# Optimization experiments

Measured on AMD Instinct MI355X. Metric: run time of the kernel, lower is better.

Reference implementation:

```python
import jax, jax.numpy as jnp
import numpy as np

NH, WS, SS = 8, 7, 3  # num_heads, window_size, shift_size
EPS = 1e-5


def _rel_pos_index(ws):
    coords = np.stack(np.meshgrid(np.arange(ws), np.arange(ws), indexing='ij'))
    coords = coords.reshape(2, -1)                      # [2, L]
    rel = coords[:, :, None] - coords[:, None, :]       # [2, L, L]
    rel = rel.transpose(1, 2, 0) + (ws - 1)
    return rel[..., 0] * (2 * ws - 1) + rel[..., 1]     # [L, L] int


def _attn_mask(H, W, ws, ss):
    # region labels for shifted-window masking (torchvision semantics)
    img = np.zeros((H, W))
    slices = (slice(0, -ws), slice(-ws, -ss), slice(-ss, None))
    cnt = 0
    for hs in slices:
        for wsl in slices:
            img[hs, wsl] = cnt
            cnt += 1
    win = img.reshape(H // ws, ws, W // ws, ws).transpose(0, 2, 1, 3).reshape(-1, ws * ws)
    mask = (win[:, None, :] != win[:, :, None]).astype(np.float32) * (-100.0)
    return mask  # [nWin, L, L]


def _layernorm(x, gamma, beta):
    mu = jnp.mean(x, axis=-1, keepdims=True)
    var = jnp.mean(jnp.square(x - mu), axis=-1, keepdims=True)
    return (x - mu) * jax.lax.rsqrt(var + EPS) * gamma + beta


def _swin_attention(x, qkv_w, qkv_b, proj_w, proj_b, rpb_table):
    B, H, W, C = x.shape
    HD = C // NH
    L = WS * WS
    nH, nW = H // WS, W // WS
    # cyclic shift
    xs = jnp.roll(x, shift=(-SS, -SS), axis=(1, 2))
    # window partition -> [B*nWin, L, C]
    xw = xs.reshape(B, nH, WS, nW, WS, C).transpose(0, 1, 3, 2, 4, 5).reshape(B * nH * nW, L, C)
    qkv = jnp.einsum('nlc,dc->nld', xw, qkv_w) + qkv_b
    qkv = qkv.reshape(-1, L, 3, NH, HD).transpose(2, 0, 3, 1, 4)  # [3, N, h, L, d]
    q, k, v = qkv[0] * (HD ** -0.5), qkv[1], qkv[2]
    attn = jnp.einsum('nhid,nhjd->nhij', q, k)  # [N, h, L, L]
    bias = rpb_table[jnp.asarray(_rel_pos_index(WS))]  # [L, L, h]
    attn = attn + bias.transpose(2, 0, 1)[None]
    mask = jnp.asarray(_attn_mask(H, W, WS, SS))  # [nWin, L, L]
    nwin = nH * nW
    attn = attn.reshape(B, nwin, NH, L, L) + mask[None, :, None]
    attn = jax.nn.softmax(attn.reshape(-1, NH, L, L), axis=-1)
    out = jnp.einsum('nhij,nhjd->nhid', attn, v).transpose(0, 2, 1, 3).reshape(-1, L, C)
    out = jnp.einsum('nlc,dc->nld', out, proj_w) + proj_b
    # reverse windows and shift
    out = out.reshape(B, nH, nW, WS, WS, C).transpose(0, 1, 3, 2, 4, 5).reshape(B, H, W, C)
    return jnp.roll(out, shift=(SS, SS), axis=(1, 2))


def setup_inputs() -> dict:
    key = jax.random.key(0)
    ks = jax.random.split(key, 8)
    B, H, W, C = 32, 56, 56, 256
    F = 4 * C
    s = 0.02
    return {
        'x': jax.random.normal(ks[0], (B, H, W, C), jnp.float32),
        'qkv_w': jax.random.normal(ks[1], (3 * C, C), jnp.float32) * s,
        'qkv_b': jnp.zeros((3 * C,), jnp.float32),
        'proj_w': jax.random.normal(ks[2], (C, C), jnp.float32) * s,
        'proj_b': jnp.zeros((C,), jnp.float32),
        'rpb_table': jax.random.normal(ks[3], ((2 * WS - 1) ** 2, NH), jnp.float32) * s,
        'gamma1': jnp.ones((C,), jnp.float32),
        'beta1': jnp.zeros((C,), jnp.float32),
        'w1': jax.random.normal(ks[4], (C, F), jnp.float32) * s,
        'b1': jax.random.normal(ks[5], (F,), jnp.float32) * 1e-6,
        'w2': jax.random.normal(ks[6], (F, C), jnp.float32) * s,
        'b2': jax.random.normal(ks[7], (C,), jnp.float32) * 1e-6,
        'gamma2': jnp.ones((C,), jnp.float32),
        'beta2': jnp.zeros((C,), jnp.float32),
    }


def reference(x, qkv_w, qkv_b, proj_w, proj_b, rpb_table, gamma1, beta1, w1, b1, w2, b2, gamma2, beta2):
    # post-norm residual block: x + norm1(attn(x)); x + norm2(mlp(x))
    a = _swin_attention(x, qkv_w, qkv_b, proj_w, proj_b, rpb_table)
    x = x + _layernorm(a, gamma1, beta1)
    h = jax.nn.gelu(jnp.einsum('bhwc,cf->bhwf', x, w1) + b1, approximate=False)
    m = jnp.einsum('bhwf,fc->bhwc', h, w2) + b2
    x = x + _layernorm(m, gamma2, beta2)
    return x
```

## Files before the change

### kernel.cpp

```cpp
#include <hip/hip_runtime.h>
#include <hip/hip_bf16.h>


typedef unsigned short ushort_t;
typedef short bf16x8 __attribute__((ext_vector_type(8)));
typedef float f32x4 __attribute__((ext_vector_type(4)));

#define WAITV0 asm volatile("s_waitcnt vmcnt(0)" ::: "memory")
#define WAITV3 asm volatile("s_waitcnt vmcnt(3)" ::: "memory")
#define WAITV4 asm volatile("s_waitcnt vmcnt(4)" ::: "memory")
#define WAITV5 asm volatile("s_waitcnt vmcnt(5)" ::: "memory")
#define WAITL0 asm volatile("s_waitcnt lgkmcnt(0)" ::: "memory")
#define BAR    __builtin_amdgcn_s_barrier()

__device__ __forceinline__ float bf2f(unsigned short u) {
    union { unsigned int i; float f; } x; x.i = ((unsigned int)u) << 16; return x.f;
}
__device__ __forceinline__ unsigned short f2bf(float f) {
    union { float f; unsigned int i; } x; x.f = f;
    unsigned int r = x.i + 0x7fffu + ((x.i >> 16) & 1u);
    return (unsigned short)(r >> 16);
}
__device__ __forceinline__ bf16x8 pack8(float4 a, float4 b) {
    bf16x8 r;
    r[0] = (short)f2bf(a.x); r[1] = (short)f2bf(a.y);
    r[2] = (short)f2bf(a.z); r[3] = (short)f2bf(a.w);
    r[4] = (short)f2bf(b.x); r[5] = (short)f2bf(b.y);
    r[6] = (short)f2bf(b.z); r[7] = (short)f2bf(b.w);
    return r;
}
__device__ __forceinline__ void gl_lds16(const ushort_t* g, ushort_t* l) {
    __builtin_amdgcn_global_load_lds((const __attribute__((address_space(1))) void*)g,
                                     (__attribute__((address_space(3))) void*)l, 16, 0, 0);
}
__device__ __forceinline__ float gelu_f(float v) {
    float s = v * 0.70710678118654752f;
    float ax = fabsf(s);
    float t = __builtin_amdgcn_rcpf(1.0f + 0.3275911f * ax);
    float poly = ((((1.061405429f * t - 1.453152027f) * t + 1.421413741f) * t
                   - 0.284496736f) * t + 0.254829592f) * t;
    float y = 1.0f - poly * __expf(-ax * ax);
    float e = (s < 0.f) ? -y : y;
    return 0.5f * v * (1.0f + e);
}

__device__ __forceinline__ long swin_src_off(int m) {
    int n = m / 49, l = m - n * 49;
    int b = n >> 6, win = n & 63;
    int wh = win >> 3, ww = win & 7;
    int i = l / 7, j = l - i * 7;
    int hs = wh * 7 + i + 3; if (hs >= 56) hs -= 56;
    int ws = ww * 7 + j + 3; if (ws >= 56) ws -= 56;
    return ((long)(b * 56 + hs) * 56 + ws) * 256;
}

template<int SRCT>
__global__ __launch_bounds__(256)
void convW(const float* __restrict__ src, ushort_t* __restrict__ dst, int N, int kshift)
{
    int idx = blockIdx.x * 256 + threadIdx.x;
    int kk = idx & ((1 << kshift) - 1), nn = idx >> kshift;
    float v = SRCT ? src[(long)kk * N + nn] : src[idx];
    dst[idx] = f2bf(v);
}

template<int ACT, int AMODE, int NCOLS>
__global__ __launch_bounds__(512)
void gemmW(const void* __restrict__ Av, const ushort_t* __restrict__ W,
           const float* __restrict__ bias, ushort_t* __restrict__ C,
           int M, int N, int K)
{
    constexpr int NA = (AMODE == 1) ? 2 : 3;
    __shared__ ushort_t As[NA * 4096];
    __shared__ ushort_t Bs[3 * 8192];
    const int t = threadIdx.x, lane = t & 63, w = t >> 6;
    const int cpx = gridDim.x >> 3;
    const int wg = (blockIdx.x & 7) * cpx + (blockIdx.x >> 3);
    const int row0 = (wg / NCOLS) * 128, col0 = (wg % NCOLS) * 256;
    const int wm = (w >> 2) * 64, wn = (w & 3) * 64;

    const int ra = t >> 2, sa = ((t & 3) ^ ((ra >> 1) & 3)) * 8;
    const ushort_t* ag = nullptr;
    const float* axr = nullptr;
    if (AMODE == 0) ag = (const ushort_t*)Av + (long)(row0 + ra) * K + sa;
    else            axr = (const float*)Av + swin_src_off(row0 + ra) + sa;

    const int ub0 = t, ub1 = t + 512;
    const int rb0 = ub0 >> 2, sb0 = ((ub0 & 3) ^ ((rb0 >> 1) & 3)) * 8;
    const int rb1 = ub1 >> 2, sb1 = ((ub1 & 3) ^ ((rb1 >> 1) & 3)) * 8;
    const ushort_t* bg0 = W + (long)(col0 + rb0) * K + sb0;
    const ushort_t* bg1 = W + (long)(col0 + rb1) * K + sb1;

    int offA[4], offB[4];
    #pragma unroll
    for (int i = 0; i < 4; i++) {
        int r2 = wm + i * 16 + (lane & 15);
        offA[i] = r2 * 32 + (((lane >> 4) ^ ((r2 >> 1) & 3)) * 8);
        int r3 = wn + i * 16 + (lane & 15);
        offB[i] = r3 * 32 + (((lane >> 4) ^ ((r3 >> 1) & 3)) * 8);
    }

    f32x4 acc[4][4] = {};
    float4 va0, vb0, va1, vb1;

    if (AMODE == 0) {
        gl_lds16(ag,      &As[t * 8]);
        gl_lds16(bg0,      &Bs[ub0 * 8]);
        gl_lds16(bg1,      &Bs[ub1 * 8]);
        gl_lds16(ag + 32, &As[4096 + t * 8]);
        gl_lds16(bg0 + 32, &Bs[8192 + ub0 * 8]);
        gl_lds16(bg1 + 32, &Bs[8192 + ub1 * 8]);
        WAITV3; BAR;
    } else {
        va0 = *(const float4*)axr;        vb0 = *(const float4*)(axr + 4);
        gl_lds16(bg0,      &Bs[ub0 * 8]);
        gl_lds16(bg1,      &Bs[ub1 * 8]);
        va1 = *(const float4*)(axr + 32); vb1 = *(const float4*)(axr + 36);
        gl_lds16(bg0 + 32, &Bs[8192 + ub0 * 8]);
        gl_lds16(bg1 + 32, &Bs[8192 + ub1 * 8]);
        WAITV4;
        *(bf16x8*)&As[t * 8] = pack8(va0, vb0);
        WAITL0; BAR;
    }

    const int nk = K >> 5;
    int i0 = 0, i1 = 1, i2 = 2;
    for (int kt = 0; kt < nk; kt++) {
        const bool more = (kt + 2 < nk);
        if (more) {
            const int k2 = (kt + 2) * 32;
            if (AMODE == 0) {
                gl_lds16(ag + k2, &As[i2 * 4096 + t * 8]);
            } else {
                if (kt & 1) { va1 = *(const float4*)(axr + k2); vb1 = *(const float4*)(axr + k2 + 4); }
                else        { va0 = *(const float4*)(axr + k2); vb0 = *(const float4*)(axr + k2 + 4); }
            }
            gl_lds16(bg0 + k2, &Bs[i2 * 8192 + ub0 * 8]);
            gl_lds16(bg1 + k2, &Bs[i2 * 8192 + ub1 * 8]);
        }
        {
            const int abase = (AMODE == 1 ? (kt & 1) : i0) * 4096;
            const int bbase = i0 * 8192;
            bf16x8 af[4], bw[4];
            #pragma unroll
            for (int i = 0; i < 4; i++) {
                af[i] = *(const bf16x8*)&As[abase + offA[i]];
                bw[i] = *(const bf16x8*)&Bs[bbase + offB[i]];
            }
            #pragma unroll
            for (int mi = 0; mi < 4; mi++)
                #pragma unroll
                for (int ni = 0; ni < 4; ni++)
                    acc[mi][ni] = __builtin_amdgcn_mfma_f32_16x16x32_bf16(af[mi], bw[ni], acc[mi][ni], 0, 0, 0);
        }
        if (kt < nk - 1) {
            if (AMODE == 0) {
                if (more) { WAITV3; } else { WAITV0; }
            } else {
                if (more) { WAITV4; } else { WAITV0; }
                if (kt & 1) *(bf16x8*)&As[t * 8]        = pack8(va0, vb0);
                else        *(bf16x8*)&As[4096 + t * 8] = pack8(va1, vb1);
                WAITL0;
            }
            BAR;
        }
        int tmp = i0; i0 = i1; i1 = i2; i2 = tmp;
    }

    #pragma unroll
    for (int mi = 0; mi < 4; mi++)
        #pragma unroll
        for (int ni = 0; ni < 4; ni++) {
            const int c = col0 + wn + ni * 16 + (lane & 15);
            const float bv = bias[c];
            #pragma unroll
            for (int r = 0; r < 4; r++) {
                const int rr = row0 + wm + mi * 16 + (lane >> 4) * 4 + r;
                float v = acc[mi][ni][r] + bv;
                if (ACT) v = gelu_f(v);
                C[(long)rr * N + c] = f2bf(v);
            }
        }
}

__global__ __launch_bounds__(64)
void attn_mfma(const ushort_t* __restrict__ qkv, const float* __restrict__ rpb,
               ushort_t* __restrict__ out)
{
    __shared__ ushort_t v_t[32 * 72];
    __shared__ ushort_t p_lds[64 * 72];
    __shared__ float bias_s[169];

    const int blk = blockIdx.x;
    const int n = blk >> 3, h = blk & 7;
    const int l = threadIdx.x;
    const long wbase = (long)n * 49 * 768 + h * 32;
    const float scale = 0.17677669529663687f;

    {
        int j = min(l, 48);
        const ushort_t* vr = qkv + wbase + (long)j * 768 + 512;
        #pragma unroll
        for (int c = 0; c < 4; c++) {
            bf16x8 vv = *(const bf16x8*)(vr + c * 8);
            #pragma unroll
            for (int e = 0; e < 8; e++) v_t[(c * 8 + e) * 72 + l] = (ushort_t)vv[e];
        }
    }
    for (int idx = l; idx < 169; idx += 64) bias_s[idx] = rpb[idx * 8 + h];
    __syncthreads();

    f32x4 s[4][4] = {};
    {
        bf16x8 aq[4], bk[4];
        #pragma unroll
        for (int mt = 0; mt < 4; mt++) {
            int i = min(mt * 16 + (l & 15), 48);
            aq[mt] = *(const bf16x8*)(qkv + wbase + (long)i * 768 + (l >> 4) * 8);
        }
        #pragma unroll
        for (int nt = 0; nt < 4; nt++) {
            int j = min(nt * 16 + (l & 15), 48);
            bk[nt] = *(const bf16x8*)(qkv + wbase + (long)j * 768 + 256 + (l >> 4) * 8);
        }
        #pragma unroll
        for (int mt = 0; mt < 4; mt++)
            #pragma unroll
            for (int nt = 0; nt < 4; nt++)
                s[mt][nt] = __builtin_amdgcn_mfma_f32_16x16x32_bf16(aq[mt], bk[nt], s[mt][nt], 0, 0, 0);
    }

    const int win = n & 63, wh = win >> 3, ww = win & 7;
    int yj[4], xj[4], regj[4]; bool jv[4];
    #pragma unroll
    for (int nt = 0; nt < 4; nt++) {
        int j = nt * 16 + (l & 15);
        jv[nt] = (j <= 48);
        int jc = min(j, 48);
        yj[nt] = jc / 7; xj[nt] = jc - yj[nt] * 7;
        int hs = wh * 7 + yj[nt], wsx = ww * 7 + xj[nt];
        regj[nt] = (hs < 49 ? 0 : (hs < 53 ? 1 : 2)) * 3 + (wsx < 49 ? 0 : (wsx < 53 ? 1 : 2));
    }
    float rinv[4][4];
    #pragma unroll
    for (int mt = 0; mt < 4; mt++) {
        #pragma unroll
        for (int r = 0; r < 4; r++) {
            int i = mt * 16 + (l >> 4) * 4 + r;
            int ic = min(i, 48);
            int yi = ic / 7, xi = ic - yi * 7;
            int hs = wh * 7 + yi, wsx = ww * 7 + xi;
            int regi = (hs < 49 ? 0 : (hs < 53 ? 1 : 2)) * 3 + (wsx < 49 ? 0 : (wsx < 53 ? 1 : 2));
            float val[4];
            #pragma unroll
            for (int nt = 0; nt < 4; nt++) {
                float v = s[mt][nt][r] * scale + bias_s[(yi - yj[nt] + 6) * 13 + (xi - xj[nt] + 6)];
                if (regi != regj[nt]) v -= 100.f;
                val[nt] = jv[nt] ? v : -1e30f;
            }
            float mx = fmaxf(fmaxf(val[0], val[1]), fmaxf(val[2], val[3]));
            #pragma unroll
            for (int off = 1; off <= 8; off <<= 1) mx = fmaxf(mx, __shfl_xor(mx, off));
            float sum = 0.f;
            #pragma unroll
            for (int nt = 0; nt < 4; nt++) { val[nt] = __expf(val[nt] - mx); sum += val[nt]; }
            #pragma unroll
            for (int off = 1; off <= 8; off <<= 1) sum += __shfl_xor(sum, off);
            rinv[mt][r] = 1.0f / sum;
            #pragma unroll
            for (int nt = 0; nt < 4; nt++)
                p_lds[i * 72 + nt * 16 + (l & 15)] = f2bf(val[nt]);
        }
    }
    __syncthreads();

    f32x4 o[4][2] = {};
    #pragma unroll
    for (int ks = 0; ks < 2; ks++) {
        bf16x8 pa[4], vb[2];
        #pragma unroll
        for (int mt = 0; mt < 4; mt++)
            pa[mt] = *(const bf16x8*)&p_lds[(mt * 16 + (l & 15)) * 72 + ks * 32 + (l >> 4) * 8];
        #pragma unroll
        for (int nt = 0; nt < 2; nt++)
            vb[nt] = *(const bf16x8*)&v_t[(nt * 16 + (l & 15)) * 72 + ks * 32 + (l >> 4) * 8];
        #pragma unroll
        for (int mt = 0; mt < 4; mt++)
            #pragma unroll
            for (int nt = 0; nt < 2; nt++)
                o[mt][nt] = __builtin_amdgcn_mfma_f32_16x16x32_bf16(pa[mt], vb[nt], o[mt][nt], 0, 0, 0);
    }
    #pragma unroll
    for (int mt = 0; mt < 4; mt++)
        #pragma unroll
        for (int r = 0; r < 4; r++) {
            int i = mt * 16 + (l >> 4) * 4 + r;
            if (i < 49) {
                float rs = rinv[mt][r];
                #pragma unroll
                for (int nt = 0; nt < 2; nt++) {
                    int d = nt * 16 + (l & 15);
                    out[((long)n * 49 + i) * 256 + h * 32 + d] = f2bf(o[mt][nt][r] * rs);
                }
            }
        }
}

__global__ __launch_bounds__(512)
void projln1(const ushort_t* __restrict__ A, const ushort_t* __restrict__ W,
             const float* __restrict__ pb, const float* __restrict__ x,
             const float* __restrict__ gamma, const float* __restrict__ beta,
             ushort_t* __restrict__ x1b)
{
    __shared__ ushort_t As[3 * 4096];
    __shared__ ushort_t Bs[3 * 8192];
    __shared__ float red_s[128][4];
    __shared__ float red_ss[128][4];
    __shared__ int srow_s[128];
    const int t = threadIdx.x, lane = t & 63, w = t >> 6;
    const int row0 = blockIdx.x * 128;
    const int wm = (w >> 2) * 64, wn = (w & 3) * 64;

    if (t < 128) srow_s[t] = (int)(swin_src_off(row0 + t) >> 8);

    const int ra0 = t >> 2, sa0 = ((t & 3) ^ ((ra0 >> 1) & 3)) * 8;
    const ushort_t* ag = A + (long)(row0 + ra0) * 256 + sa0;
    const int ub0 = t, ub1 = t + 512;
    const int rb0 = ub0 >> 2, sb0 = ((ub0 & 3) ^ ((rb0 >> 1) & 3)) * 8;
    const int rb1 = ub1 >> 2, sb1 = ((ub1 & 3) ^ ((rb1 >> 1) & 3)) * 8;
    const ushort_t* bg0 = W + (long)rb0 * 256 + sb0;
    const ushort_t* bg1 = W + (long)rb1 * 256 + sb1;

    int offA[4], offB[4];
    #pragma unroll
    for (int i = 0; i < 4; i++) {
        int ra = wm + i * 16 + (lane & 15);
        offA[i] = ra * 32 + (((lane >> 4) ^ ((ra >> 1) & 3)) * 8);
        int rb = wn + i * 16 + (lane & 15);
        offB[i] = rb * 32 + (((lane >> 4) ^ ((rb >> 1) & 3)) * 8);
    }

    f32x4 acc[4][4] = {};
    gl_lds16(ag,       &As[t * 8]);
    gl_lds16(bg0,       &Bs[ub0 * 8]);
    gl_lds16(bg1,       &Bs[ub1 * 8]);
    gl_lds16(ag + 32,  &As[4096 + t * 8]);
    gl_lds16(bg0 + 32,  &Bs[8192 + ub0 * 8]);
    gl_lds16(bg1 + 32,  &Bs[8192 + ub1 * 8]);
    WAITV3; BAR;

    int i0 = 0, i1 = 1, i2 = 2;
    for (int kt = 0; kt < 8; kt++) {
        const bool more = (kt + 2 < 8);
        if (more) {
            const int k2 = (kt + 2) * 32;
            gl_lds16(ag + k2, &As[i2 * 4096 + t * 8]);
            gl_lds16(bg0 + k2, &Bs[i2 * 8192 + ub0 * 8]);
            gl_lds16(bg1 + k2, &Bs[i2 * 8192 + ub1 * 8]);
        }
        bf16x8 af[4], bw[4];
        #pragma unroll
        for (int i = 0; i < 4; i++) {
            af[i] = *(const bf16x8*)&As[i0 * 4096 + offA[i]];
            bw[i] = *(const bf16x8*)&Bs[i0 * 8192 + offB[i]];
        }
        #pragma unroll
        for (int mi = 0; mi < 4; mi++)
            #pragma unroll
            for (int ni = 0; ni < 4; ni++)
                acc[mi][ni] = __builtin_amdgcn_mfma_f32_16x16x32_bf16(af[mi], bw[ni], acc[mi][ni], 0, 0, 0);
        if (kt < 7) {
            if (more) { WAITV3; } else { WAITV0; }
            BAR;
        }
        int tmp = i0; i0 = i1; i1 = i2; i2 = tmp;
    }

    float pbv[4], g1v[4], be1v[4];
    #pragma unroll
    for (int ni = 0; ni < 4; ni++) {
        int col = wn + ni * 16 + (lane & 15);
        pbv[ni] = pb[col]; g1v[ni] = gamma[col]; be1v[ni] = beta[col];
    }
    #pragma unroll
    for (int mi = 0; mi < 4; mi++)
        #pragma unroll
        for (int rr = 0; rr < 4; rr++) {
            float s = 0.f, ss = 0.f;
            #pragma unroll
            for (int ni = 0; ni < 4; ni++) {
                float v = acc[mi][ni][rr] + pbv[ni];
                acc[mi][ni][rr] = v; s += v; ss += v * v;
            }
            #pragma unroll
            for (int off = 1; off <= 8; off <<= 1) { s += __shfl_xor(s, off); ss += __shfl_xor(ss, off); }
            if ((lane & 15) == 0) {
                int r = wm + mi * 16 + (lane >> 4) * 4 + rr;
                red_s[r][w & 3] = s; red_ss[r][w & 3] = ss;
            }
        }
    __syncthreads();
    #pragma unroll
    for (int mi = 0; mi < 4; mi++)
        #pragma unroll
        for (int rr = 0; rr < 4; rr++) {
            const int r = wm + mi * 16 + (lane >> 4) * 4 + rr;
            const float s = red_s[r][0] + red_s[r][1] + red_s[r][2] + red_s[r][3];
            const float ss = red_ss[r][0] + red_ss[r][1] + red_ss[r][2] + red_ss[r][3];
            const float mu = s * (1.0f / 256.0f);
            const float rstd = rsqrtf(ss * (1.0f / 256.0f) - mu * mu + 1e-5f);
            const long sp = srow_s[r];
            #pragma unroll
            for (int ni = 0; ni < 4; ni++) {
                int col = wn + ni * 16 + (lane & 15);
                float o = x[sp * 256 + col] + (acc[mi][ni][rr] - mu) * rstd * g1v[ni] + be1v[ni];
                x1b[sp * 256 + col] = f2bf(o);
            }
        }
}

__global__ __launch_bounds__(256)
void mlp2ln2(const ushort_t* __restrict__ A, const ushort_t* __restrict__ W,
             const float* __restrict__ pb, const ushort_t* __restrict__ x1res,
             const float* __restrict__ gamma, const float* __restrict__ beta,
             float* __restrict__ out)
{
    __shared__ ushort_t As[3 * 2048];
    __shared__ ushort_t Bs[3 * 8192];
    __shared__ float red_s[64][4];
    __shared__ float red_ss[64][4];
    const int t = threadIdx.x, lane = t & 63, w = t >> 6;
    const int row0 = blockIdx.x * 64;
    const int wn = w * 64;

    const int ra0 = t >> 2, sa0 = ((t & 3) ^ ((ra0 >> 1) & 3)) * 8;
    const ushort_t* ag = A + (long)(row0 + ra0) * 1024 + sa0;
    const ushort_t* bg[4];
    int ub[4];
    #pragma unroll
    for (int i = 0; i < 4; i++) {
        ub[i] = t + i * 256;
        int rb = ub[i] >> 2, sb = ((ub[i] & 3) ^ ((rb >> 1) & 3)) * 8;
        bg[i] = W + (long)rb * 1024 + sb;
    }

    int offA[4], offB[4];
    #pragma unroll
    for (int i = 0; i < 4; i++) {
        int ra = i * 16 + (lane & 15);
        offA[i] = ra * 32 + (((lane >> 4) ^ ((ra >> 1) & 3)) * 8);
        int rb = wn + i * 16 + (lane & 15);
        offB[i] = rb * 32 + (((lane >> 4) ^ ((rb >> 1) & 3)) * 8);
    }

    f32x4 acc[4][4] = {};
    gl_lds16(ag,      &As[t * 8]);
    #pragma unroll
    for (int i = 0; i < 4; i++) gl_lds16(bg[i],      &Bs[ub[i] * 8]);
    gl_lds16(ag + 32, &As[2048 + t * 8]);
    #pragma unroll
    for (int i = 0; i < 4; i++) gl_lds16(bg[i] + 32, &Bs[8192 + ub[i] * 8]);
    WAITV5; BAR;

    int i0 = 0, i1 = 1, i2 = 2;
    for (int kt = 0; kt < 32; kt++) {
        const bool more = (kt + 2 < 32);
        if (more) {
            const int k2 = (kt + 2) * 32;
            gl_lds16(ag + k2, &As[i2 * 2048 + t * 8]);
            #pragma unroll
            for (int i = 0; i < 4; i++) gl_lds16(bg[i] + k2, &Bs[i2 * 8192 + ub[i] * 8]);
        }
        bf16x8 af[4], bw[4];
        #pragma unroll
        for (int i2x = 0; i2x < 4; i2x++) {
            af[i2x] = *(const bf16x8*)&As[i0 * 2048 + offA[i2x]];
            bw[i2x] = *(const bf16x8*)&Bs[i0 * 8192 + offB[i2x]];
        }
        #pragma unroll
        for (int mi = 0; mi < 4; mi++)
            #pragma unroll
            for (int ni = 0; ni < 4; ni++)
                acc[mi][ni] = __builtin_amdgcn_mfma_f32_16x16x32_bf16(af[mi], bw[ni], acc[mi][ni], 0, 0, 0);
        if (kt < 31) {
            if (more) { WAITV5; } else { WAITV0; }
            BAR;
        }
        int tmp = i0; i0 = i1; i1 = i2; i2 = tmp;
    }

    float pbv[4], g2v[4], be2v[4];
    #pragma unroll
    for (int ni = 0; ni < 4; ni++) {
        int col = wn + ni * 16 + (lane & 15);
        pbv[ni] = pb[col]; g2v[ni] = gamma[col]; be2v[ni] = beta[col];
    }
    #pragma unroll
    for (int mi = 0; mi < 4; mi++)
        #pragma unroll
        for (int rr = 0; rr < 4; rr++) {
            float s = 0.f, ss = 0.f;
            #pragma unroll
            for (int ni = 0; ni < 4; ni++) {
                float v = acc[mi][ni][rr] + pbv[ni];
                acc[mi][ni][rr] = v; s += v; ss += v * v;
            }
            #pragma unroll
            for (int off = 1; off <= 8; off <<= 1) { s += __shfl_xor(s, off); ss += __shfl_xor(ss, off); }
            if ((lane & 15) == 0) {
                int r = mi * 16 + (lane >> 4) * 4 + rr;
                red_s[r][w] = s; red_ss[r][w] = ss;
            }
        }
    __syncthreads();
    #pragma unroll
    for (int mi = 0; mi < 4; mi++)
        #pragma unroll
        for (int rr = 0; rr < 4; rr++) {
            const int r = mi * 16 + (lane >> 4) * 4 + rr;
            const float s = red_s[r][0] + red_s[r][1] + red_s[r][2] + red_s[r][3];
            const float ss = red_ss[r][0] + red_ss[r][1] + red_ss[r][2] + red_ss[r][3];
            const float mu = s * (1.0f / 256.0f);
            const float rstd = rsqrtf(ss * (1.0f / 256.0f) - mu * mu + 1e-5f);
            const long gr = row0 + r;
            #pragma unroll
            for (int ni = 0; ni < 4; ni++) {
                int col = wn + ni * 16 + (lane & 15);
                out[gr * 256 + col] = bf2f(x1res[gr * 256 + col])
                                    + (acc[mi][ni][rr] - mu) * rstd * g2v[ni] + be2v[ni];
            }
        }
}

extern "C" void kernel_launch(void* const* d_in, const int* in_sizes, int n_in,
                              void* d_out, int out_size, void* d_ws, size_t ws_size,
                              hipStream_t stream) {
    const float* x      = (const float*)d_in[0];
    const float* qkv_w  = (const float*)d_in[1];
    const float* qkv_b  = (const float*)d_in[2];
    const float* proj_w = (const float*)d_in[3];
    const float* proj_b = (const float*)d_in[4];
    const float* rpb    = (const float*)d_in[5];
    const float* gamma1 = (const float*)d_in[6];
    const float* beta1  = (const float*)d_in[7];
    const float* w1     = (const float*)d_in[8];
    const float* b1     = (const float*)d_in[9];
    const float* w2     = (const float*)d_in[10];
    const float* b2     = (const float*)d_in[11];
    const float* gamma2 = (const float*)d_in[12];
    const float* beta2  = (const float*)d_in[13];
    float* outf = (float*)d_out;

    ushort_t* attnout = (ushort_t*)d_out;

    char* ws = (char*)d_ws;
    ushort_t* qkvb  = (ushort_t*)ws;
    ushort_t* hbuf  = (ushort_t*)ws;
    ushort_t* x1b   = (ushort_t*)(ws + 154140672ULL);
    ushort_t* wqkvb = (ushort_t*)(ws + 205520896ULL);
    ushort_t* wprojb= (ushort_t*)(ws + 205914112ULL);
    ushort_t* w1t   = (ushort_t*)(ws + 206045184ULL);
    ushort_t* w2t   = (ushort_t*)(ws + 206569472ULL);

    const int M = 100352, MC = 50176;
    dim3 blk(256);
    convW<0><<<dim3(768),  blk, 0, stream>>>(qkv_w,  wqkvb,  768,  8);
    convW<0><<<dim3(256),  blk, 0, stream>>>(proj_w, wprojb, 256,  8);
    convW<1><<<dim3(1024), blk, 0, stream>>>(w1,     w1t,    1024, 8);
    convW<1><<<dim3(1024), blk, 0, stream>>>(w2,     w2t,    256, 10);
    gemmW<0, 1, 3><<<dim3(2352), dim3(512), 0, stream>>>(x, wqkvb, qkv_b, qkvb, M, 768, 256);
    attn_mfma<<<dim3(16384), dim3(64), 0, stream>>>(qkvb, rpb, attnout);
    projln1<<<dim3(784), dim3(512), 0, stream>>>(attnout, wprojb, proj_b, x,
                                                 gamma1, beta1, x1b);
    for (int c2 = 0; c2 < 2; c2++) {
        const long off = (long)c2 * MC * 256;
        gemmW<1, 0, 4><<<dim3(1568), dim3(512), 0, stream>>>(x1b + off, w1t, b1, hbuf, MC, 1024, 256);
        mlp2ln2<<<dim3(784), blk, 0, stream>>>(hbuf, w2t, b2, x1b + off,
                                               gamma2, beta2, outf + off);
    }
}
```

Before: 529.4 us.

## Merge weight conversions, add 128x128 MLP1 GEMM, double-buffer mlp2, set MFMA priority

The four weight-conversion launches become one kernel. The two-chunk MLP loop becomes a single pass over all rows, using a new 256-thread 128x128-tile GEMM for fc1+GELU. mlp2ln2 moves from triple to double buffering with a full vmcnt(0) wait each step. s_setprio is raised around the MFMA blocks in all GEMMs. The workspace is re-laid out so the full hidden buffer fits, which needs a larger workspace, and the shallower pipeline may expose more load latency.

```diff
diff --git a/kernel.cpp b/kernel.cpp
--- a/kernel.cpp
+++ b/kernel.cpp
@@ -9,9 +9,10 @@
 #define WAITV0 asm volatile("s_waitcnt vmcnt(0)" ::: "memory")
 #define WAITV3 asm volatile("s_waitcnt vmcnt(3)" ::: "memory")
 #define WAITV4 asm volatile("s_waitcnt vmcnt(4)" ::: "memory")
-#define WAITV5 asm volatile("s_waitcnt vmcnt(5)" ::: "memory")
 #define WAITL0 asm volatile("s_waitcnt lgkmcnt(0)" ::: "memory")
 #define BAR    __builtin_amdgcn_s_barrier()
+#define PRIO1  __builtin_amdgcn_s_setprio(1)
+#define PRIO0  __builtin_amdgcn_s_setprio(0)
 
 __device__ __forceinline__ float bf2f(unsigned short u) {
     union { unsigned int i; float f; } x; x.i = ((unsigned int)u) << 16; return x.f;
@@ -54,14 +55,28 @@
     return ((long)(b * 56 + hs) * 56 + ws) * 256;
 }
 
-template<int SRCT>
 __global__ __launch_bounds__(256)
-void convW(const float* __restrict__ src, ushort_t* __restrict__ dst, int N, int kshift)
+void convAll(const float* __restrict__ qkv_w, const float* __restrict__ proj_w,
+             const float* __restrict__ w1, const float* __restrict__ w2,
+             ushort_t* __restrict__ dq, ushort_t* __restrict__ dp,
+             ushort_t* __restrict__ d1, ushort_t* __restrict__ d2)
 {
-    int idx = blockIdx.x * 256 + threadIdx.x;
-    int kk = idx & ((1 << kshift) - 1), nn = idx >> kshift;
-    float v = SRCT ? src[(long)kk * N + nn] : src[idx];
-    dst[idx] = f2bf(v);
+    int b = blockIdx.x, tix = threadIdx.x;
+    if (b < 768) {
+        int idx = b * 256 + tix;
+        dq[idx] = f2bf(qkv_w[idx]);
+    } else if (b < 1024) {
+        int idx = (b - 768) * 256 + tix;
+        dp[idx] = f2bf(proj_w[idx]);
+    } else if (b < 2048) {
+        int idx = (b - 1024) * 256 + tix;
+        int kk = idx & 255, nn = idx >> 8;
+        d1[idx] = f2bf(w1[(long)kk * 1024 + nn]);
+    } else {
+        int idx = (b - 2048) * 256 + tix;
+        int kk = idx & 1023, nn = idx >> 10;
+        d2[idx] = f2bf(w2[(long)kk * 256 + nn]);
+    }
 }
 
 template<int ACT, int AMODE, int NCOLS>
@@ -147,11 +162,13 @@
                 af[i] = *(const bf16x8*)&As[abase + offA[i]];
                 bw[i] = *(const bf16x8*)&Bs[bbase + offB[i]];
             }
+            PRIO1;
             #pragma unroll
             for (int mi = 0; mi < 4; mi++)
                 #pragma unroll
                 for (int ni = 0; ni < 4; ni++)
                     acc[mi][ni] = __builtin_amdgcn_mfma_f32_16x16x32_bf16(af[mi], bw[ni], acc[mi][ni], 0, 0, 0);
+            PRIO0;
         }
         if (kt < nk - 1) {
             if (AMODE == 0) {
@@ -167,6 +184,93 @@
         int tmp = i0; i0 = i1; i1 = i2; i2 = tmp;
     }
 
+    #pragma unroll
+    for (int mi = 0; mi < 4; mi++)
+        #pragma unroll
+        for (int ni = 0; ni < 4; ni++) {
+            const int c = col0 + wn + ni * 16 + (lane & 15);
+            const float bv = bias[c];
+            #pragma unroll
+            for (int r = 0; r < 4; r++) {
+                const int rr = row0 + wm + mi * 16 + (lane >> 4) * 4 + r;
+                float v = acc[mi][ni][r] + bv;
+                if (ACT) v = gelu_f(v);
+                C[(long)rr * N + c] = f2bf(v);
+            }
+        }
+}
+
+template<int ACT, int NCOLS>
+__global__ __launch_bounds__(256)
+void gemm128(const ushort_t* __restrict__ A, const ushort_t* __restrict__ W,
+             const float* __restrict__ bias, ushort_t* __restrict__ C,
+             int M, int N, int K)
+{
+    __shared__ ushort_t As[2][128 * 32];
+    __shared__ ushort_t Bs[2][128 * 32];
+    const int t = threadIdx.x, lane = t & 63, wave = t >> 6;
+    const int cpx = gridDim.x >> 3;
+    const int wg = (blockIdx.x & 7) * cpx + (blockIdx.x >> 3);
+    const int row0 = (wg / NCOLS) * 128, col0 = (wg % NCOLS) * 128;
+    const int wm = (wave >> 1) * 64, wn = (wave & 1) * 64;
+
+    const int u0 = t, u1 = t + 256;
+    const int r0 = u0 >> 2, s0 = ((u0 & 3) ^ ((r0 >> 1) & 3)) * 8;
+    const int r1 = u1 >> 2, s1 = ((u1 & 3) ^ ((r1 >> 1) & 3)) * 8;
+    const ushort_t* a0 = A + (long)(row0 + r0) * K + s0;
+    const ushort_t* a1 = A + (long)(row0 + r1) * K + s1;
+    const ushort_t* b0 = W + (long)(col0 + r0) * K + s0;
+    const ushort_t* b1 = W + (long)(col0 + r1) * K + s1;
+
+    int offA[4], offB[4];
+    #pragma unroll
+    for (int i = 0; i < 4; i++) {
+        int ra = wm + i * 16 + (lane & 15);
+        offA[i] = ra * 32 + (((lane >> 4) ^ ((ra >> 1) & 3)) * 8);
+        int rb = wn + i * 16 + (lane & 15);
+        offB[i] = rb * 32 + (((lane >> 4) ^ ((rb >> 1) & 3)) * 8);
+    }
+
+    f32x4 acc[4][4] = {};
+    gl_lds16(a0, &As[0][u0 * 8]); gl_lds16(a1, &As[0][u1 * 8]);
+    gl_lds16(b0, &Bs[0][u0 * 8]); gl_lds16(b1, &Bs[0][u1 * 8]);
+    WAITV0; BAR;
+    const int nk = K >> 5;
+    for (int kt = 0; kt < nk - 1; kt++) {
+        const int cur = kt & 1, nxt = cur ^ 1, k1 = (kt + 1) * 32;
+        gl_lds16(a0 + k1, &As[nxt][u0 * 8]); gl_lds16(a1 + k1, &As[nxt][u1 * 8]);
+        gl_lds16(b0 + k1, &Bs[nxt][u0 * 8]); gl_lds16(b1 + k1, &Bs[nxt][u1 * 8]);
+        bf16x8 af[4], bw[4];
+        #pragma unroll
+        for (int i = 0; i < 4; i++) {
+            af[i] = *(const bf16x8*)&As[cur][offA[i]];
+            bw[i] = *(const bf16x8*)&Bs[cur][offB[i]];
+        }
+        PRIO1;
+        #pragma unroll
+        for (int mi = 0; mi < 4; mi++)
+            #pragma unroll
+            for (int ni = 0; ni < 4; ni++)
+                acc[mi][ni] = __builtin_amdgcn_mfma_f32_16x16x32_bf16(af[mi], bw[ni], acc[mi][ni], 0, 0, 0);
+        PRIO0;
+        WAITV0; BAR;
+    }
+    {
+        const int cur = (nk - 1) & 1;
+        bf16x8 af[4], bw[4];
+        #pragma unroll
+        for (int i = 0; i < 4; i++) {
+            af[i] = *(const bf16x8*)&As[cur][offA[i]];
+            bw[i] = *(const bf16x8*)&Bs[cur][offB[i]];
+        }
+        PRIO1;
+        #pragma unroll
+        for (int mi = 0; mi < 4; mi++)
+            #pragma unroll
+            for (int ni = 0; ni < 4; ni++)
+                acc[mi][ni] = __builtin_amdgcn_mfma_f32_16x16x32_bf16(af[mi], bw[ni], acc[mi][ni], 0, 0, 0);
+        PRIO0;
+    }
     #pragma unroll
     for (int mi = 0; mi < 4; mi++)
         #pragma unroll
@@ -364,11 +468,13 @@
             af[i] = *(const bf16x8*)&As[i0 * 4096 + offA[i]];
             bw[i] = *(const bf16x8*)&Bs[i0 * 8192 + offB[i]];
         }
+        PRIO1;
         #pragma unroll
         for (int mi = 0; mi < 4; mi++)
             #pragma unroll
             for (int ni = 0; ni < 4; ni++)
                 acc[mi][ni] = __builtin_amdgcn_mfma_f32_16x16x32_bf16(af[mi], bw[ni], acc[mi][ni], 0, 0, 0);
+        PRIO0;
         if (kt < 7) {
             if (more) { WAITV3; } else { WAITV0; }
             BAR;
@@ -425,8 +531,8 @@
              const float* __restrict__ gamma, const float* __restrict__ beta,
              float* __restrict__ out)
 {
-    __shared__ ushort_t As[3 * 2048];
-    __shared__ ushort_t Bs[3 * 8192];
+    __shared__ ushort_t As[2][64 * 32];
+    __shared__ ushort_t Bs[2][256 * 32];
     __shared__ float red_s[64][4];
     __shared__ float red_ss[64][4];
     const int t = threadIdx.x, lane = t & 63, w = t >> 6;
@@ -454,41 +560,45 @@
     }
 
     f32x4 acc[4][4] = {};
-    gl_lds16(ag,      &As[t * 8]);
-    #pragma unroll
-    for (int i = 0; i < 4; i++) gl_lds16(bg[i],      &Bs[ub[i] * 8]);
-    gl_lds16(ag + 32, &As[2048 + t * 8]);
-    #pragma unroll
-    for (int i = 0; i < 4; i++) gl_lds16(bg[i] + 32, &Bs[8192 + ub[i] * 8]);
-    WAITV5; BAR;
-
-    int i0 = 0, i1 = 1, i2 = 2;
-    for (int kt = 0; kt < 32; kt++) {
-        const bool more = (kt + 2 < 32);
-        if (more) {
-            const int k2 = (kt + 2) * 32;
-            gl_lds16(ag + k2, &As[i2 * 2048 + t * 8]);
-            #pragma unroll
-            for (int i = 0; i < 4; i++) gl_lds16(bg[i] + k2, &Bs[i2 * 8192 + ub[i] * 8]);
-        }
+    gl_lds16(ag, &As[0][t * 8]);
+    #pragma unroll
+    for (int i = 0; i < 4; i++) gl_lds16(bg[i], &Bs[0][ub[i] * 8]);
+    WAITV0; BAR;
+    for (int kt = 0; kt < 31; kt++) {
+        const int cur = kt & 1, nxt = cur ^ 1, k1 = (kt + 1) * 32;
+        gl_lds16(ag + k1, &As[nxt][t * 8]);
+        #pragma unroll
+        for (int i = 0; i < 4; i++) gl_lds16(bg[i] + k1, &Bs[nxt][ub[i] * 8]);
         bf16x8 af[4], bw[4];
         #pragma unroll
-        for (int i2x = 0; i2x < 4; i2x++) {
-            af[i2x] = *(const bf16x8*)&As[i0 * 2048 + offA[i2x]];
-            bw[i2x] = *(const bf16x8*)&Bs[i0 * 8192 + offB[i2x]];
-        }
+        for (int i2 = 0; i2 < 4; i2++) {
+            af[i2] = *(const bf16x8*)&As[cur][offA[i2]];
+            bw[i2] = *(const bf16x8*)&Bs[cur][offB[i2]];
+        }
+        PRIO1;
         #pragma unroll
         for (int mi = 0; mi < 4; mi++)
             #pragma unroll
             for (int ni = 0; ni < 4; ni++)
                 acc[mi][ni] = __builtin_amdgcn_mfma_f32_16x16x32_bf16(af[mi], bw[ni], acc[mi][ni], 0, 0, 0);
-        if (kt < 31) {
-            if (more) { WAITV5; } else { WAITV0; }
-            BAR;
-        }
-        int tmp = i0; i0 = i1; i1 = i2; i2 = tmp;
-    }
-
+        PRIO0;
+        WAITV0; BAR;
+    }
+    {
+        bf16x8 af[4], bw[4];
+        #pragma unroll
+        for (int i2 = 0; i2 < 4; i2++) {
+            af[i2] = *(const bf16x8*)&As[1][offA[i2]];
+            bw[i2] = *(const bf16x8*)&Bs[1][offB[i2]];
+        }
+        PRIO1;
+        #pragma unroll
+        for (int mi = 0; mi < 4; mi++)
+            #pragma unroll
+            for (int ni = 0; ni < 4; ni++)
+                acc[mi][ni] = __builtin_amdgcn_mfma_f32_16x16x32_bf16(af[mi], bw[ni], acc[mi][ni], 0, 0, 0);
+        PRIO0;
+    }
     float pbv[4], g2v[4], be2v[4];
     #pragma unroll
     for (int ni = 0; ni < 4; ni++) {
@@ -555,27 +665,22 @@
 
     char* ws = (char*)d_ws;
     ushort_t* qkvb  = (ushort_t*)ws;
-    ushort_t* hbuf  = (ushort_t*)ws;
-    ushort_t* x1b   = (ushort_t*)(ws + 154140672ULL);
-    ushort_t* wqkvb = (ushort_t*)(ws + 205520896ULL);
-    ushort_t* wprojb= (ushort_t*)(ws + 205914112ULL);
-    ushort_t* w1t   = (ushort_t*)(ws + 206045184ULL);
-    ushort_t* w2t   = (ushort_t*)(ws + 206569472ULL);
-
-    const int M = 100352, MC = 50176;
+    ushort_t* x1b   = (ushort_t*)ws;
+    ushort_t* hbuf  = (ushort_t*)(ws + 51380224ULL);
+    ushort_t* wqkvb = (ushort_t*)(ws + 256901120ULL);
+    ushort_t* wprojb= (ushort_t*)(ws + 257294336ULL);
+    ushort_t* w1t   = (ushort_t*)(ws + 257425408ULL);
+    ushort_t* w2t   = (ushort_t*)(ws + 257949696ULL);
+
+    const int M = 100352;
     dim3 blk(256);
-    convW<0><<<dim3(768),  blk, 0, stream>>>(qkv_w,  wqkvb,  768,  8);
-    convW<0><<<dim3(256),  blk, 0, stream>>>(proj_w, wprojb, 256,  8);
-    convW<1><<<dim3(1024), blk, 0, stream>>>(w1,     w1t,    1024, 8);
-    convW<1><<<dim3(1024), blk, 0, stream>>>(w2,     w2t,    256, 10);
+    convAll<<<dim3(3072), blk, 0, stream>>>(qkv_w, proj_w, w1, w2,
+                                            wqkvb, wprojb, w1t, w2t);
     gemmW<0, 1, 3><<<dim3(2352), dim3(512), 0, stream>>>(x, wqkvb, qkv_b, qkvb, M, 768, 256);
     attn_mfma<<<dim3(16384), dim3(64), 0, stream>>>(qkvb, rpb, attnout);
     projln1<<<dim3(784), dim3(512), 0, stream>>>(attnout, wprojb, proj_b, x,
                                                  gamma1, beta1, x1b);
-    for (int c2 = 0; c2 < 2; c2++) {
-        const long off = (long)c2 * MC * 256;
-        gemmW<1, 0, 4><<<dim3(1568), dim3(512), 0, stream>>>(x1b + off, w1t, b1, hbuf, MC, 1024, 256);
-        mlp2ln2<<<dim3(784), blk, 0, stream>>>(hbuf, w2t, b2, x1b + off,
-                                               gamma2, beta2, outf + off);
-    }
-}
+    gemm128<1, 8><<<dim3(6272), blk, 0, stream>>>(x1b, w1t, b1, hbuf, M, 1024, 256);
+    mlp2ln2<<<dim3(1568), blk, 0, stream>>>(hbuf, w2t, b2, x1b,
+                                            gamma2, beta2, outf);
+}
```

Result: no change. 527.0 us (-0.5%).
